# Kernel tuning notes

Hardware: AMD Instinct MI355X
Metric: run time of the kernel (lower is better)

Reference implementation:

```python
import jax, jax.numpy as jnp
import numpy as np

B, C, H, W = 4, 3, 512, 512
V, NF = 12000, 24000
UH, UW = 1024, 1024


def setup_inputs() -> dict:
    key = jax.random.key(0)
    ks = jax.random.split(key, 8)
    img = jax.random.normal(ks[0], (B, C, H, W), jnp.float32)
    mesh = jax.random.normal(ks[1], (B, V, 3), jnp.float32) * 0.3
    mesh = mesh.at[:, :, 2].add(3.0)  # keep depth positive so projection is well-defined
    face = jax.random.randint(ks[2], (NF, 3), 0, V, jnp.int32)
    focal = 800.0 + 200.0 * jax.random.uniform(ks[3], (B, 2), jnp.float32)
    princpt = jnp.tile(jnp.array([[W / 2.0, H / 2.0]], jnp.float32), (B, 1))
    R = jnp.tile(jnp.eye(3, dtype=jnp.float32)[None], (B, 1, 1))
    t = jnp.zeros((B, 3), jnp.float32)
    # pytorch3d packed convention: face id f of batch i is stored as f + NF*i, background = -1
    base = jax.random.randint(ks[4], (B, H, W), -1, NF, jnp.int32)
    offs = (NF * jnp.arange(B, dtype=jnp.int32))[:, None, None]
    pix_to_face_xy = jnp.where(base != -1, base + offs, -1)
    pix_to_face_uv = jax.random.randint(ks[5], (UH, UW), -1, NF, jnp.int32)
    bary = jax.random.uniform(ks[6], (UH, UW, 3), jnp.float32) + 1e-3
    bary_coords_uv = bary / bary.sum(-1, keepdims=True)
    return dict(img=img, mesh=mesh, face=face, focal=focal, princpt=princpt,
                R=R, t=t, pix_to_face_xy=pix_to_face_xy,
                pix_to_face_uv=pix_to_face_uv, bary_coords_uv=bary_coords_uv)


def _grid_sample(img, grid):
    # F.grid_sample: bilinear, align_corners=True, zero padding.
    # img [B,C,H,W], grid [B,Uh,Uw,2] in [-1,1] -> out [B,C,Uh,Uw]
    Bq, Cq, Hq, Wq = img.shape
    ix = (grid[..., 0] + 1.0) * 0.5 * (Wq - 1)
    iy = (grid[..., 1] + 1.0) * 0.5 * (Hq - 1)
    ix0 = jnp.floor(ix)
    iy0 = jnp.floor(iy)
    wx1 = ix - ix0
    wx0 = 1.0 - wx1
    wy1 = iy - iy0
    wy0 = 1.0 - wy1
    bidx = jnp.arange(Bq)[:, None, None]

    def tap(yf, xf, w):
        valid = (xf >= 0) & (xf <= Wq - 1) & (yf >= 0) & (yf <= Hq - 1)
        xi = jnp.clip(xf, 0, Wq - 1).astype(jnp.int32)
        yi = jnp.clip(yf, 0, Hq - 1).astype(jnp.int32)
        vals = img[bidx, :, yi, xi]  # [B,Uh,Uw,C]
        return vals * (w * valid)[..., None]

    out = (tap(iy0, ix0, wy0 * wx0) + tap(iy0, ix0 + 1.0, wy0 * wx1)
           + tap(iy0 + 1.0, ix0, wy1 * wx0) + tap(iy0 + 1.0, ix0 + 1.0, wy1 * wx1))
    return jnp.transpose(out, (0, 3, 1, 2))


def _forward(img, mesh, focal, princpt, R, t, bary_coords_uv,
             face, pix_to_face_xy, pix_to_face_uv):
    Bq, Cq, Hq, Wq = img.shape
    Fn = face.shape[0]
    Vn = mesh.shape[1]
    # camera transform + perspective projection
    mesh_cam = jnp.einsum('bij,bvj->bvi', R, mesh) + t[:, None, :]
    x = mesh_cam[..., 0] / mesh_cam[..., 2] * focal[:, None, 0] + princpt[:, None, 0]
    y = mesh_cam[..., 1] / mesh_cam[..., 2] * focal[:, None, 1] + princpt[:, None, 1]
    mesh_img = jnp.stack((x, y), 2)  # [B,V,2]
    # per-batch visible-face mask (packed ids: subtract Fn*i; torch's index -1 wraps
    # to face Fn-1 when scattering 1.0 -- replicate that exactly)
    local = jnp.where(pix_to_face_xy != -1,
                      pix_to_face_xy - Fn * jnp.arange(Bq, dtype=pix_to_face_xy.dtype)[:, None, None],
                      -1)
    local = jnp.where(local < 0, local + Fn, local)
    valid = jnp.zeros((Bq, Fn), jnp.float32).at[
        jnp.arange(Bq)[:, None], local.reshape(Bq, -1)].set(1.0)
    # invalidate invisible faces: vertex ids -> -1
    faces_b = jnp.where(valid[:, :, None] > 0, face[None].astype(jnp.int32), -1)  # [B,F,3]
    puv = jnp.where(pix_to_face_uv < 0, pix_to_face_uv + Fn, pix_to_face_uv)  # wrap like torch
    vidx = faces_b[:, puv, :]  # [B,UH,UW,3]
    invisible = (vidx[..., 0] == -1).astype(img.dtype)  # [B,UH,UW]
    vw = jnp.where(vidx < 0, vidx + Vn, vidx)  # -1 wraps to last vertex, like torch
    gathered = mesh_img[jnp.arange(Bq)[:, None, None, None], vw]  # [B,UH,UW,3,2]
    uvpos = jnp.einsum('bhwkc,hwk->bhwc', gathered, bary_coords_uv)  # barycentric blend
    grid = jnp.stack((uvpos[..., 0] / (Wq - 1) * 2.0 - 1.0,
                      uvpos[..., 1] / (Hq - 1) * 2.0 - 1.0), -1)
    uvmap = _grid_sample(img, grid)  # [B,C,UH,UW]
    uvmap = jnp.where((pix_to_face_uv == -1)[None, None], -1.0, uvmap)
    uvmap = uvmap * (1.0 - invisible)[:, None] - invisible[:, None]
    return uvmap


def reference(img, mesh, face, focal, princpt, R, t,
              pix_to_face_xy, pix_to_face_uv, bary_coords_uv):
    return _forward(img, mesh, focal, princpt, R, t, bary_coords_uv,
                    face, pix_to_face_xy, pix_to_face_uv)
```

## Files before the change

kernel.cpp:

```cpp
#include <hip/hip_runtime.h>

#define BQ 4
#define CQ 3
#define HQ 512
#define WQ 512
#define VN 12000
#define FN 24000
#define UHN 1024
#define UWN 1024
#define IMGPLANE (HQ * WQ)

#define MESHIMG_OFF 0u
#define VALID_OFF   384000u
#define FD_OFF      480000u
#define IMGI_OFF    3552000u
#define WS_NEED     (IMGI_OFF + (size_t)BQ * HQ * WQ * 4 * sizeof(float))

__global__ void init_kernel(const float* __restrict__ mesh,
                            const float* __restrict__ focal,
                            const float* __restrict__ princpt,
                            const float* __restrict__ R,
                            const float* __restrict__ t,
                            float* __restrict__ mesh_img,
                            unsigned int* __restrict__ valid_u32) {
    int idx = blockIdx.x * blockDim.x + threadIdx.x;
    if (idx < (BQ * FN) / 4) valid_u32[idx] = 0u;
    if (idx >= BQ * VN) return;
    int b = idx / VN;
    const float* Rb = R + b * 9;
    const float* tb = t + b * 3;
    float mx = mesh[idx * 3 + 0];
    float my = mesh[idx * 3 + 1];
    float mz = mesh[idx * 3 + 2];
    float cx = Rb[0] * mx + Rb[1] * my + Rb[2] * mz + tb[0];
    float cy = Rb[3] * mx + Rb[4] * my + Rb[5] * mz + tb[1];
    float cz = Rb[6] * mx + Rb[7] * my + Rb[8] * mz + tb[2];
    float x = cx / cz * focal[b * 2 + 0] + princpt[b * 2 + 0];
    float y = cy / cz * focal[b * 2 + 1] + princpt[b * 2 + 1];
    mesh_img[idx * 2 + 0] = x;
    mesh_img[idx * 2 + 1] = y;
}

__global__ void interleave_kernel(const float* __restrict__ img,
                                  float4* __restrict__ img_i) {
    int idx = blockIdx.x * blockDim.x + threadIdx.x;
    if (idx >= BQ * HQ * WQ) return;
    int b = idx >> 18;
    int p = idx & (IMGPLANE - 1);
    const float* ib = img + (size_t)b * CQ * IMGPLANE + p;
    float4 v;
    v.x = ib[0];
    v.y = ib[IMGPLANE];
    v.z = ib[2 * IMGPLANE];
    v.w = 0.0f;
    img_i[idx] = v;
}

__global__ void valid_kernel(const int4* __restrict__ ptf_xy4,
                             unsigned char* __restrict__ valid_t) {
    int i = blockIdx.x * blockDim.x + threadIdx.x;
    if (i >= (BQ * HQ * WQ) / 4) return;
    int b = (i * 4) >> 18;
    int4 p4 = ptf_xy4[i];
    int p[4] = {p4.x, p4.y, p4.z, p4.w};
#pragma unroll
    for (int k = 0; k < 4; ++k) {
        int l = (p[k] != -1) ? (p[k] - FN * b) : -1;
        if (l < 0) l += FN;
        valid_t[l * BQ + b] = 1;
    }
}

__global__ void fd_kernel(const int* __restrict__ face,
                          const float* __restrict__ mesh_img,
                          const unsigned char* __restrict__ valid_t,
                          float4* __restrict__ fd) {
    int idx = blockIdx.x * blockDim.x + threadIdx.x;
    if (idx >= FN * BQ) return;
    int f = idx >> 2;
    int b = idx & 3;
    int v0 = face[f * 3 + 0];
    int v1 = face[f * 3 + 1];
    int v2 = face[f * 3 + 2];
    const float* mi = mesh_img + (size_t)b * VN * 2;
    float4 a, c;
    a.x = mi[v0 * 2 + 0]; a.y = mi[v0 * 2 + 1];
    a.z = mi[v1 * 2 + 0]; a.w = mi[v1 * 2 + 1];
    c.x = mi[v2 * 2 + 0]; c.y = mi[v2 * 2 + 1];
    c.z = valid_t[f * BQ + b] ? 1.0f : 0.0f;
    c.w = 0.0f;
    fd[idx * 2 + 0] = a;
    fd[idx * 2 + 1] = c;
}

__global__ void uv_kernel(const float4* __restrict__ img_i,
                          const float4* __restrict__ fd,
                          const int* __restrict__ ptf_uv,
                          const float* __restrict__ bary,
                          float* __restrict__ out) {
    int idx = blockIdx.x * blockDim.x + threadIdx.x;
    if (idx >= UHN * UWN) return;

    const size_t PLANE = (size_t)UHN * UWN;

    int puv = ptf_uv[idx];
    if (puv == -1) {
#pragma unroll
        for (int b = 0; b < BQ; ++b) {
            float* ob = out + (size_t)b * CQ * PLANE + idx;
            __builtin_nontemporal_store(-1.0f, ob);
            __builtin_nontemporal_store(-1.0f, ob + PLANE);
            __builtin_nontemporal_store(-1.0f, ob + 2 * PLANE);
        }
        return;
    }
    int pu = (puv < 0) ? puv + FN : puv;

    const float4* fdp = fd + (size_t)pu * 8;
    float4 fa[BQ], fc[BQ];
#pragma unroll
    for (int b = 0; b < BQ; ++b) {
        fa[b] = fdp[2 * b + 0];
        fc[b] = fdp[2 * b + 1];
    }

    float w0 = bary[idx * 3 + 0];
    float w1 = bary[idx * 3 + 1];
    float w2 = bary[idx * 3 + 2];

#pragma unroll
    for (int b = 0; b < BQ; ++b) {
        float* ob = out + (size_t)b * CQ * PLANE + idx;
        if (fc[b].z == 0.0f) {
            __builtin_nontemporal_store(-1.0f, ob);
            __builtin_nontemporal_store(-1.0f, ob + PLANE);
            __builtin_nontemporal_store(-1.0f, ob + 2 * PLANE);
            continue;
        }
        float ux = w0 * fa[b].x + w1 * fa[b].z + w2 * fc[b].x;
        float uy = w0 * fa[b].y + w1 * fa[b].w + w2 * fc[b].y;

        float gx = ux / (float)(WQ - 1) * 2.0f - 1.0f;
        float gy = uy / (float)(HQ - 1) * 2.0f - 1.0f;
        float ix = (gx + 1.0f) * 0.5f * (float)(WQ - 1);
        float iy = (gy + 1.0f) * 0.5f * (float)(HQ - 1);

        float ix0 = floorf(ix), iy0 = floorf(iy);
        float wx1 = ix - ix0, wx0 = 1.0f - wx1;
        float wy1 = iy - iy0, wy0 = 1.0f - wy1;

        float xf[2] = {ix0, ix0 + 1.0f};
        float yf[2] = {iy0, iy0 + 1.0f};
        float wx[2] = {wx0, wx1};
        float wy[2] = {wy0, wy1};

        const float4* ibi = img_i + (size_t)b * IMGPLANE;
        float acc0 = 0.f, acc1 = 0.f, acc2 = 0.f;
#pragma unroll
        for (int ty = 0; ty < 2; ++ty) {
#pragma unroll
            for (int tx = 0; tx < 2; ++tx) {
                float wgt = wy[ty] * wx[tx];
                bool ok = (xf[tx] >= 0.0f) && (xf[tx] <= (float)(WQ - 1)) &&
                          (yf[ty] >= 0.0f) && (yf[ty] <= (float)(HQ - 1));
                float wv = ok ? wgt : 0.0f;
                int xi = (int)fminf(fmaxf(xf[tx], 0.0f), (float)(WQ - 1));
                int yi = (int)fminf(fmaxf(yf[ty], 0.0f), (float)(HQ - 1));
                float4 v = ibi[yi * WQ + xi];
                acc0 += v.x * wv;
                acc1 += v.y * wv;
                acc2 += v.z * wv;
            }
        }
        __builtin_nontemporal_store(acc0, ob);
        __builtin_nontemporal_store(acc1, ob + PLANE);
        __builtin_nontemporal_store(acc2, ob + 2 * PLANE);
    }
}

__global__ void uv_kernel_fb(const float* __restrict__ img,
                             const int* __restrict__ face,
                             const unsigned char* __restrict__ valid_t,
                             const float* __restrict__ mesh_img,
                             const int* __restrict__ ptf_uv,
                             const float* __restrict__ bary,
                             float* __restrict__ out) {
    int idx = blockIdx.x * blockDim.x + threadIdx.x;
    if (idx >= UHN * UWN) return;
    const size_t PLANE = (size_t)UHN * UWN;
    int puv = ptf_uv[idx];
    if (puv == -1) {
#pragma unroll
        for (int b = 0; b < BQ; ++b) {
            float* ob = out + (size_t)b * CQ * PLANE + idx;
            __builtin_nontemporal_store(-1.0f, ob);
            __builtin_nontemporal_store(-1.0f, ob + PLANE);
            __builtin_nontemporal_store(-1.0f, ob + 2 * PLANE);
        }
        return;
    }
    int pu = (puv < 0) ? puv + FN : puv;
    unsigned int vmask = *(const unsigned int*)(valid_t + (size_t)pu * BQ);
    float w0 = bary[idx * 3 + 0];
    float w1 = bary[idx * 3 + 1];
    float w2 = bary[idx * 3 + 2];
    int v0 = face[pu * 3 + 0];
    int v1 = face[pu * 3 + 1];
    int v2 = face[pu * 3 + 2];
#pragma unroll
    for (int b = 0; b < BQ; ++b) {
        float* ob = out + (size_t)b * CQ * PLANE + idx;
        bool vis = ((vmask >> (8 * b)) & 0xffu) != 0u;
        if (!vis) {
            __builtin_nontemporal_store(-1.0f, ob);
            __builtin_nontemporal_store(-1.0f, ob + PLANE);
            __builtin_nontemporal_store(-1.0f, ob + 2 * PLANE);
            continue;
        }
        const float* mi = mesh_img + (size_t)b * VN * 2;
        float ux = w0 * mi[v0 * 2 + 0] + w1 * mi[v1 * 2 + 0] + w2 * mi[v2 * 2 + 0];
        float uy = w0 * mi[v0 * 2 + 1] + w1 * mi[v1 * 2 + 1] + w2 * mi[v2 * 2 + 1];
        float gx = ux / (float)(WQ - 1) * 2.0f - 1.0f;
        float gy = uy / (float)(HQ - 1) * 2.0f - 1.0f;
        float ix = (gx + 1.0f) * 0.5f * (float)(WQ - 1);
        float iy = (gy + 1.0f) * 0.5f * (float)(HQ - 1);
        float ix0 = floorf(ix), iy0 = floorf(iy);
        float wx1 = ix - ix0, wx0 = 1.0f - wx1;
        float wy1 = iy - iy0, wy0 = 1.0f - wy1;
        float xf[2] = {ix0, ix0 + 1.0f};
        float yf[2] = {iy0, iy0 + 1.0f};
        float wx[2] = {wx0, wx1};
        float wy[2] = {wy0, wy1};
        float acc0 = 0.f, acc1 = 0.f, acc2 = 0.f;
        const float* ib = img + (size_t)b * CQ * IMGPLANE;
#pragma unroll
        for (int ty = 0; ty < 2; ++ty) {
#pragma unroll
            for (int tx = 0; tx < 2; ++tx) {
                float wgt = wy[ty] * wx[tx];
                bool ok = (xf[tx] >= 0.0f) && (xf[tx] <= (float)(WQ - 1)) &&
                          (yf[ty] >= 0.0f) && (yf[ty] <= (float)(HQ - 1));
                float wv = ok ? wgt : 0.0f;
                int xi = (int)fminf(fmaxf(xf[tx], 0.0f), (float)(WQ - 1));
                int yi = (int)fminf(fmaxf(yf[ty], 0.0f), (float)(HQ - 1));
                const float* ip = ib + yi * WQ + xi;
                acc0 += ip[0] * wv;
                acc1 += ip[IMGPLANE] * wv;
                acc2 += ip[2 * IMGPLANE] * wv;
            }
        }
        __builtin_nontemporal_store(acc0, ob);
        __builtin_nontemporal_store(acc1, ob + PLANE);
        __builtin_nontemporal_store(acc2, ob + 2 * PLANE);
    }
}

extern "C" void kernel_launch(void* const* d_in, const int* in_sizes, int n_in,
                              void* d_out, int out_size, void* d_ws, size_t ws_size,
                              hipStream_t stream) {
    const float* img     = (const float*)d_in[0];
    const float* mesh    = (const float*)d_in[1];
    const int*   face    = (const int*)d_in[2];
    const float* focal   = (const float*)d_in[3];
    const float* princpt = (const float*)d_in[4];
    const float* R       = (const float*)d_in[5];
    const float* t       = (const float*)d_in[6];
    const int*   ptf_xy  = (const int*)d_in[7];
    const int*   ptf_uv  = (const int*)d_in[8];
    const float* bary    = (const float*)d_in[9];
    float* out = (float*)d_out;

    unsigned char* ws = (unsigned char*)d_ws;
    float*         mesh_img = (float*)(ws + MESHIMG_OFF);
    unsigned char* valid_t  = ws + VALID_OFF;
    float4*        fd       = (float4*)(ws + FD_OFF);
    float4*        img_i    = (float4*)(ws + IMGI_OFF);

    init_kernel<<<(BQ * VN + 255) / 256, 256, 0, stream>>>(
        mesh, focal, princpt, R, t, mesh_img, (unsigned int*)valid_t);

    valid_kernel<<<((BQ * HQ * WQ / 4) + 255) / 256, 256, 0, stream>>>(
        (const int4*)ptf_xy, valid_t);

    if (ws_size >= WS_NEED) {
        interleave_kernel<<<(BQ * HQ * WQ + 255) / 256, 256, 0, stream>>>(img, img_i);

        fd_kernel<<<(FN * BQ + 255) / 256, 256, 0, stream>>>(
            face, mesh_img, valid_t, fd);

        uv_kernel<<<(UHN * UWN + 255) / 256, 256, 0, stream>>>(
            img_i, fd, ptf_uv, bary, out);
    } else {
        uv_kernel_fb<<<(UHN * UWN + 255) / 256, 256, 0, stream>>>(
            img, face, valid_t, mesh_img, ptf_uv, bary, out);
    }
}
```

Measured before the change: 200.6 us.

## Split UV sampling per batch across blocks and fuse interleave with visibility marking

The uv kernel now gives each thread one (pixel, batch) pair instead of looping over all four batches. Block indices interleave batches so neighbouring blocks reuse the same ptf_uv and bary lines from cache. The face data table becomes batch-major to match. The interleave and valid-marking kernels merge into one vectorized prep kernel that reads float4 rows, which removes a launch and improves load width. The trade-off is that ptf_uv and bary are now re-read once per batch, and the fallback path now calls prep_kernel, which writes img_i even when the workspace may be too small.

```diff
diff --git a/kernel.cpp b/kernel.cpp
--- a/kernel.cpp
+++ b/kernel.cpp
@@ -41,31 +41,30 @@
     mesh_img[idx * 2 + 1] = y;
 }
 
-__global__ void interleave_kernel(const float* __restrict__ img,
-                                  float4* __restrict__ img_i) {
-    int idx = blockIdx.x * blockDim.x + threadIdx.x;
-    if (idx >= BQ * HQ * WQ) return;
-    int b = idx >> 18;
-    int p = idx & (IMGPLANE - 1);
-    const float* ib = img + (size_t)b * CQ * IMGPLANE + p;
-    float4 v;
-    v.x = ib[0];
-    v.y = ib[IMGPLANE];
-    v.z = ib[2 * IMGPLANE];
-    v.w = 0.0f;
-    img_i[idx] = v;
-}
-
-__global__ void valid_kernel(const int4* __restrict__ ptf_xy4,
-                             unsigned char* __restrict__ valid_t) {
+__global__ void prep_kernel(const float* __restrict__ img,
+                            float4* __restrict__ img_i,
+                            const int4* __restrict__ ptf_xy4,
+                            unsigned char* __restrict__ valid_t) {
     int i = blockIdx.x * blockDim.x + threadIdx.x;
     if (i >= (BQ * HQ * WQ) / 4) return;
-    int b = (i * 4) >> 18;
+    int g = i * 4;
+    int b = g >> 18;
+    int p = g & (IMGPLANE - 1);
+
+    const float* ib = img + (size_t)b * CQ * IMGPLANE + p;
+    float4 r0 = *(const float4*)(ib);
+    float4 r1 = *(const float4*)(ib + IMGPLANE);
+    float4 r2 = *(const float4*)(ib + 2 * IMGPLANE);
+    img_i[g + 0] = make_float4(r0.x, r1.x, r2.x, 0.0f);
+    img_i[g + 1] = make_float4(r0.y, r1.y, r2.y, 0.0f);
+    img_i[g + 2] = make_float4(r0.z, r1.z, r2.z, 0.0f);
+    img_i[g + 3] = make_float4(r0.w, r1.w, r2.w, 0.0f);
+
     int4 p4 = ptf_xy4[i];
-    int p[4] = {p4.x, p4.y, p4.z, p4.w};
+    int pv[4] = {p4.x, p4.y, p4.z, p4.w};
 #pragma unroll
     for (int k = 0; k < 4; ++k) {
-        int l = (p[k] != -1) ? (p[k] - FN * b) : -1;
+        int l = (pv[k] != -1) ? (pv[k] - FN * b) : -1;
         if (l < 0) l += FN;
         valid_t[l * BQ + b] = 1;
     }
@@ -77,8 +76,8 @@
                           float4* __restrict__ fd) {
     int idx = blockIdx.x * blockDim.x + threadIdx.x;
     if (idx >= FN * BQ) return;
-    int f = idx >> 2;
-    int b = idx & 3;
+    int b = idx / FN;
+    int f = idx - b * FN;
     int v0 = face[f * 3 + 0];
     int v1 = face[f * 3 + 1];
     int v2 = face[f * 3 + 2];
@@ -89,8 +88,8 @@
     c.x = mi[v2 * 2 + 0]; c.y = mi[v2 * 2 + 1];
     c.z = valid_t[f * BQ + b] ? 1.0f : 0.0f;
     c.w = 0.0f;
-    fd[idx * 2 + 0] = a;
-    fd[idx * 2 + 1] = c;
+    fd[(size_t)idx * 2 + 0] = a;
+    fd[(size_t)idx * 2 + 1] = c;
 }
 
 __global__ void uv_kernel(const float4* __restrict__ img_i,
@@ -98,84 +97,76 @@
                           const int* __restrict__ ptf_uv,
                           const float* __restrict__ bary,
                           float* __restrict__ out) {
-    int idx = blockIdx.x * blockDim.x + threadIdx.x;
-    if (idx >= UHN * UWN) return;
+    int blk = blockIdx.x;
+    int r = blk & 7;
+    int b = r >> 1;
+    int pixBlk = ((blk >> 3) << 1) | (r & 1);
+    int idx = pixBlk * 256 + threadIdx.x;
 
     const size_t PLANE = (size_t)UHN * UWN;
+    float* ob = out + (size_t)b * CQ * PLANE + idx;
 
     int puv = ptf_uv[idx];
     if (puv == -1) {
-#pragma unroll
-        for (int b = 0; b < BQ; ++b) {
-            float* ob = out + (size_t)b * CQ * PLANE + idx;
-            __builtin_nontemporal_store(-1.0f, ob);
-            __builtin_nontemporal_store(-1.0f, ob + PLANE);
-            __builtin_nontemporal_store(-1.0f, ob + 2 * PLANE);
-        }
+        __builtin_nontemporal_store(-1.0f, ob);
+        __builtin_nontemporal_store(-1.0f, ob + PLANE);
+        __builtin_nontemporal_store(-1.0f, ob + 2 * PLANE);
         return;
     }
     int pu = (puv < 0) ? puv + FN : puv;
 
-    const float4* fdp = fd + (size_t)pu * 8;
-    float4 fa[BQ], fc[BQ];
-#pragma unroll
-    for (int b = 0; b < BQ; ++b) {
-        fa[b] = fdp[2 * b + 0];
-        fc[b] = fdp[2 * b + 1];
+    const float4* fdp = fd + ((size_t)b * FN + pu) * 2;
+    float4 fa = fdp[0];
+    float4 fc = fdp[1];
+    if (fc.z == 0.0f) {
+        __builtin_nontemporal_store(-1.0f, ob);
+        __builtin_nontemporal_store(-1.0f, ob + PLANE);
+        __builtin_nontemporal_store(-1.0f, ob + 2 * PLANE);
+        return;
     }
 
     float w0 = bary[idx * 3 + 0];
     float w1 = bary[idx * 3 + 1];
     float w2 = bary[idx * 3 + 2];
 
-#pragma unroll
-    for (int b = 0; b < BQ; ++b) {
-        float* ob = out + (size_t)b * CQ * PLANE + idx;
-        if (fc[b].z == 0.0f) {
-            __builtin_nontemporal_store(-1.0f, ob);
-            __builtin_nontemporal_store(-1.0f, ob + PLANE);
-            __builtin_nontemporal_store(-1.0f, ob + 2 * PLANE);
-            continue;
-        }
-        float ux = w0 * fa[b].x + w1 * fa[b].z + w2 * fc[b].x;
-        float uy = w0 * fa[b].y + w1 * fa[b].w + w2 * fc[b].y;
-
-        float gx = ux / (float)(WQ - 1) * 2.0f - 1.0f;
-        float gy = uy / (float)(HQ - 1) * 2.0f - 1.0f;
-        float ix = (gx + 1.0f) * 0.5f * (float)(WQ - 1);
-        float iy = (gy + 1.0f) * 0.5f * (float)(HQ - 1);
-
-        float ix0 = floorf(ix), iy0 = floorf(iy);
-        float wx1 = ix - ix0, wx0 = 1.0f - wx1;
-        float wy1 = iy - iy0, wy0 = 1.0f - wy1;
-
-        float xf[2] = {ix0, ix0 + 1.0f};
-        float yf[2] = {iy0, iy0 + 1.0f};
-        float wx[2] = {wx0, wx1};
-        float wy[2] = {wy0, wy1};
-
-        const float4* ibi = img_i + (size_t)b * IMGPLANE;
-        float acc0 = 0.f, acc1 = 0.f, acc2 = 0.f;
-#pragma unroll
-        for (int ty = 0; ty < 2; ++ty) {
-#pragma unroll
-            for (int tx = 0; tx < 2; ++tx) {
-                float wgt = wy[ty] * wx[tx];
-                bool ok = (xf[tx] >= 0.0f) && (xf[tx] <= (float)(WQ - 1)) &&
-                          (yf[ty] >= 0.0f) && (yf[ty] <= (float)(HQ - 1));
-                float wv = ok ? wgt : 0.0f;
-                int xi = (int)fminf(fmaxf(xf[tx], 0.0f), (float)(WQ - 1));
-                int yi = (int)fminf(fmaxf(yf[ty], 0.0f), (float)(HQ - 1));
-                float4 v = ibi[yi * WQ + xi];
-                acc0 += v.x * wv;
-                acc1 += v.y * wv;
-                acc2 += v.z * wv;
-            }
-        }
-        __builtin_nontemporal_store(acc0, ob);
-        __builtin_nontemporal_store(acc1, ob + PLANE);
-        __builtin_nontemporal_store(acc2, ob + 2 * PLANE);
-    }
+    float ux = w0 * fa.x + w1 * fa.z + w2 * fc.x;
+    float uy = w0 * fa.y + w1 * fa.w + w2 * fc.y;
+
+    float gx = ux / (float)(WQ - 1) * 2.0f - 1.0f;
+    float gy = uy / (float)(HQ - 1) * 2.0f - 1.0f;
+    float ix = (gx + 1.0f) * 0.5f * (float)(WQ - 1);
+    float iy = (gy + 1.0f) * 0.5f * (float)(HQ - 1);
+
+    float ix0 = floorf(ix), iy0 = floorf(iy);
+    float wx1 = ix - ix0, wx0 = 1.0f - wx1;
+    float wy1 = iy - iy0, wy0 = 1.0f - wy1;
+
+    float xf[2] = {ix0, ix0 + 1.0f};
+    float yf[2] = {iy0, iy0 + 1.0f};
+    float wx[2] = {wx0, wx1};
+    float wy[2] = {wy0, wy1};
+
+    const float4* ibi = img_i + (size_t)b * IMGPLANE;
+    float acc0 = 0.f, acc1 = 0.f, acc2 = 0.f;
+#pragma unroll
+    for (int ty = 0; ty < 2; ++ty) {
+#pragma unroll
+        for (int tx = 0; tx < 2; ++tx) {
+            float wgt = wy[ty] * wx[tx];
+            bool ok = (xf[tx] >= 0.0f) && (xf[tx] <= (float)(WQ - 1)) &&
+                      (yf[ty] >= 0.0f) && (yf[ty] <= (float)(HQ - 1));
+            float wv = ok ? wgt : 0.0f;
+            int xi = (int)fminf(fmaxf(xf[tx], 0.0f), (float)(WQ - 1));
+            int yi = (int)fminf(fmaxf(yf[ty], 0.0f), (float)(HQ - 1));
+            float4 v = ibi[yi * WQ + xi];
+            acc0 += v.x * wv;
+            acc1 += v.y * wv;
+            acc2 += v.z * wv;
+        }
+    }
+    __builtin_nontemporal_store(acc0, ob);
+    __builtin_nontemporal_store(acc1, ob + PLANE);
+    __builtin_nontemporal_store(acc2, ob + 2 * PLANE);
 }
 
 __global__ void uv_kernel_fb(const float* __restrict__ img,
@@ -279,18 +270,17 @@
     init_kernel<<<(BQ * VN + 255) / 256, 256, 0, stream>>>(
         mesh, focal, princpt, R, t, mesh_img, (unsigned int*)valid_t);
 
-    valid_kernel<<<((BQ * HQ * WQ / 4) + 255) / 256, 256, 0, stream>>>(
-        (const int4*)ptf_xy, valid_t);
-
     if (ws_size >= WS_NEED) {
-        interleave_kernel<<<(BQ * HQ * WQ + 255) / 256, 256, 0, stream>>>(img, img_i);
+        prep_kernel<<<((BQ * HQ * WQ / 4) + 255) / 256, 256, 0, stream>>>(
+            img, img_i, (const int4*)ptf_xy, valid_t);
 
         fd_kernel<<<(FN * BQ + 255) / 256, 256, 0, stream>>>(
             face, mesh_img, valid_t, fd);
 
-        uv_kernel<<<(UHN * UWN + 255) / 256, 256, 0, stream>>>(
-            img_i, fd, ptf_uv, bary, out);
+        uv_kernel<<<16384, 256, 0, stream>>>(img_i, fd, ptf_uv, bary, out);
     } else {
+        prep_kernel<<<((BQ * HQ * WQ / 4) + 255) / 256, 256, 0, stream>>>(
+            img, img_i, (const int4*)ptf_xy, valid_t);
         uv_kernel_fb<<<(UHN * UWN + 255) / 256, 256, 0, stream>>>(
             img, face, valid_t, mesh_img, ptf_uv, bary, out);
     }
```

Measured after the change: 214.8 us. 1.07x slower.
